# Optimization experiments

Measured on AMD Instinct MI355X. Metric: run time of the kernel, lower is better.

The kernel has to match this reference:

```python
import jax, jax.numpy as jnp
import numpy as np
from jax import lax

B, C, H, W = 8, 64, 96, 96
OC = 64
KH = KW = 3
DG = 1
STRIDE = 1
PAD = 1
DIL = 1


def setup_inputs() -> dict:
    key = jax.random.key(0)
    k1, k2, k3, k4, k5 = jax.random.split(key, 5)
    x = jax.random.normal(k1, (B, C, H, W), jnp.float32)
    off_ch = DG * 3 * KH * KW
    # small random offset/mask conv params (the original inits them to zero,
    # which would make offsets degenerate; small values exercise the sampler)
    w_off = jax.random.normal(k2, (off_ch, C, KH, KW), jnp.float32) * 0.01
    b_off = jax.random.normal(k3, (off_ch,), jnp.float32) * 0.01
    stdv = 1.0 / float(np.sqrt(C * KH * KW))
    weight = jax.random.uniform(k4, (OC, C, KH, KW), jnp.float32, -stdv, stdv)
    bias = jax.random.uniform(k5, (OC,), jnp.float32, -stdv, stdv)
    return {"x": x, "w_off": w_off, "b_off": b_off, "weight": weight, "bias": bias}


def _deform_conv(x, w_off, b_off, weight, bias):
    Bt, Ct, Ht, Wt = x.shape
    K = KH * KW
    # standard conv producing offsets + mask logits
    om = lax.conv_general_dilated(
        x, w_off, (STRIDE, STRIDE), ((PAD, PAD), (PAD, PAD)),
        rhs_dilation=(DIL, DIL), dimension_numbers=("NCHW", "OIHW", "NCHW"),
    ) + b_off[None, :, None, None]
    o1, o2, m = jnp.split(om, 3, axis=1)  # each [B, DG*K, Ho, Wo]
    Ho, Wo = o1.shape[2], o1.shape[3]
    mask = jax.nn.sigmoid(m).reshape(Bt, DG, 1, K, Ho, Wo)
    off_y = o1.reshape(Bt, DG, K, Ho, Wo)
    off_x = o2.reshape(Bt, DG, K, Ho, Wo)
    # base sampling grid: p = out_pos*stride - pad + k*dilation + offset
    kk = jnp.arange(K)
    base_y = (kk // KW)[:, None] * DIL + (jnp.arange(Ho) * STRIDE - PAD)[None, :]  # [K, Ho]
    base_x = (kk % KW)[:, None] * DIL + (jnp.arange(Wo) * STRIDE - PAD)[None, :]   # [K, Wo]
    py = off_y + base_y[None, None, :, :, None].astype(x.dtype)  # [B, DG, K, Ho, Wo]
    px = off_x + base_x[None, None, :, None, :].astype(x.dtype)
    y0 = jnp.floor(py)
    x0 = jnp.floor(px)
    ly = py - y0
    lx = px - x0
    Cg = Ct // DG
    xg = x.reshape(Bt, DG, Cg, Ht * Wt)

    def gath(xf, idx):  # xf [Cg, H*W], idx [K*Ho*Wo]
        return jnp.take(xf, idx, axis=1)

    gather = jax.vmap(jax.vmap(gath))  # over B, DG

    sampled = jnp.zeros((Bt, DG, Cg, K, Ho, Wo), x.dtype)
    for dy, dx, wgt in ((0, 0, (1 - ly) * (1 - lx)), (0, 1, (1 - ly) * lx),
                        (1, 0, ly * (1 - lx)), (1, 1, ly * lx)):
        yy = y0 + dy
        xx = x0 + dx
        valid = (yy >= 0) & (yy < Ht) & (xx >= 0) & (xx < Wt)
        yi = jnp.clip(yy, 0, Ht - 1).astype(jnp.int32)
        xi = jnp.clip(xx, 0, Wt - 1).astype(jnp.int32)
        idx = (yi * Wt + xi).reshape(Bt, DG, K * Ho * Wo)
        v = gather(xg, idx).reshape(Bt, DG, Cg, K, Ho, Wo)
        sampled = sampled + v * (wgt * valid)[:, :, None]
    sampled = sampled * mask  # modulated
    wr = weight.reshape(OC, DG, Cg, K)
    out = jnp.einsum("bgckhw,ogck->bohw", sampled, wr) + bias[None, :, None, None]
    return out


def reference(x, w_off, b_off, weight, bias):
    return _deform_conv(x, w_off, b_off, weight, bias)
```

## Files before the change

### kernel.cpp

```cpp
#include <hip/hip_runtime.h>
#include <math.h>

#define Bn 8
#define Cn 64
#define Hn 96
#define Wn 96
#define HWn (Hn*Wn)
#define OCn 64
#define Kn 9
#define OFFCn 27
#define NPIX (Bn*HWn)
#define PGRPS (NPIX/64)
#define BLK_PER_B (HWn/64)

#define WPK1_N 15552
#define WPK2M_SHORTS 131072
#define WS_DWORDS (WPK1_N + WPK2M_SHORTS/2)
#define WS_BYTES  ((size_t)WS_DWORDS*4)

typedef __attribute__((ext_vector_type(8))) short short8v;
typedef __attribute__((ext_vector_type(4))) float f32x4;

static __device__ __forceinline__ unsigned short bf16_rne(float f) {
    unsigned int u = __float_as_uint(f);
    return (unsigned short)((u + 0x7FFFu + ((u >> 16) & 1u)) >> 16);
}
static __device__ __forceinline__ float bf16_back(unsigned short h) {
    return __uint_as_float(((unsigned int)h) << 16);
}

__global__ __launch_bounds__(256) void dcn_wprep(
    const float* __restrict__ w_off,
    const float* __restrict__ weight,
    float* __restrict__ wpk1,
    short* __restrict__ wpk2m)
{
    const int g = blockIdx.x * 256 + threadIdx.x;
    if (g < WPK1_N) {
        const int c_all = g / 243;
        const int och   = (g % 243) / 9;
        const int ki    = g % 9;
        wpk1[g] = w_off[(och * 64 + c_all) * 9 + ki];
    }
    if (g < WPK2M_SHORTS / 8) {
        const int lane = g & 63;
        const int oct  = (g >> 6) & 3;
        const int c    = g >> 8;
        const int oc   = oct * 16 + (lane & 15);
        const float* wsrc = weight + (oc * 64 + c) * 9;
        short8v v;
#pragma unroll
        for (int j = 0; j < 8; ++j) {
            const int s = ((lane >> 4) & 3) * 8 + j;
            float f = 0.0f;
            if (s <= 8)                  f = wsrc[s];
            else if (s >= 16 && s <= 24) f = wsrc[s - 16];
            v[j] = (short)bf16_rne(f);
        }
        ((short8v*)wpk2m)[g] = v;
    }
}

__global__ __launch_bounds__(256, 2) void dcn_fused(
    const float* __restrict__ x,
    const float* __restrict__ wpk1,
    const float* __restrict__ b_off,
    const short* __restrict__ wpk2m,
    const float* __restrict__ bias,
    float* __restrict__ out)
{
    __shared__ short smp[32 * 64 * 8];
    float* lds1 = (float*)smp;

    const int tid  = threadIdx.x;
    const int lane = tid & 63;
    const int wv   = tid >> 6;
    const int cbase = __builtin_amdgcn_readfirstlane(wv * 16);

    const int bid = (blockIdx.x & 7) * BLK_PER_B + (blockIdx.x >> 3);

    const int p0  = bid * 64;
    const int b   = p0 / HWn;
    const int hwb = p0 % HWn;
    const int p   = p0 + lane;
    const int hw  = p % HWn;
    const int ho  = hw / Wn;
    const int wo  = hw % Wn;

    const float* xb = x + b * (Cn * HWn);

    float om[OFFCn];
    {
        int   toff[Kn];
        float tval[Kn];
#pragma unroll
        for (int ki = 0; ki < Kn; ++ki) {
            const int yy = ho + ki / 3 - 1, xx = wo + ki % 3 - 1;
            const bool v = (yy >= 0) && (yy < Hn) && (xx >= 0) && (xx < Wn);
            toff[ki] = min(max(yy, 0), Hn - 1) * Wn + min(max(xx, 0), Wn - 1);
            tval[ki] = v ? 1.0f : 0.0f;
        }

#pragma unroll
        for (int j = 0; j < OFFCn; ++j) om[j] = 0.0f;

        const float* wstream = wpk1 + cbase * 243;
        for (int ci = 0; ci < 16; ++ci) {
            const float* xc = xb + (cbase + ci) * HWn;
            float xk[Kn];
#pragma unroll
            for (int ki = 0; ki < Kn; ++ki)
                xk[ki] = xc[toff[ki]] * tval[ki];

            const float* wc = wstream + ci * 243;
#pragma unroll
            for (int och = 0; och < OFFCn; ++och) {
                const float* wp = wc + och * 9;
                float a = om[och];
#pragma unroll
                for (int ki = 0; ki < Kn; ++ki)
                    a = fmaf(xk[ki], wp[ki], a);
                om[och] = a;
            }
        }

#pragma unroll
        for (int j = 0; j < OFFCn; ++j)
            lds1[(wv * 64 + lane) * OFFCn + j] = om[j];
        __syncthreads();
#pragma unroll
        for (int j = 0; j < OFFCn; ++j) {
            float a = b_off[j];
#pragma unroll
            for (int ww = 0; ww < 4; ++ww)
                a += lds1[(ww * 64 + lane) * OFFCn + j];
            om[j] = a;
        }
    }

    float pw0[Kn], pw1[Kn], pw2[Kn], pw3[Kn];
    int   pav[Kn];
#pragma unroll
    for (int ki = 0; ki < Kn; ++ki) {
        const float py = om[ki]      + (float)(ki / 3 + ho - 1);
        const float px = om[Kn + ki] + (float)(ki % 3 + wo - 1);
        const float m  = 1.0f / (1.0f + __expf(-om[2 * Kn + ki]));

        const float y0f = floorf(py), x0f = floorf(px);
        const float ly = py - y0f, lx = px - x0f;
        const int iy0 = (int)y0f, ix0 = (int)x0f;
        const int iy1 = iy0 + 1,  ix1 = ix0 + 1;

        const float vy0 = (iy0 >= 0 && iy0 < Hn) ? 1.0f : 0.0f;
        const float vy1 = (iy1 >= 0 && iy1 < Hn) ? 1.0f : 0.0f;
        const float vx0 = (ix0 >= 0 && ix0 < Wn) ? 1.0f : 0.0f;
        const float vx1 = (ix1 >= 0 && ix1 < Wn) ? 1.0f : 0.0f;

        const int iy0c = min(max(iy0, 0), Hn - 1);
        const int iy1c = min(max(iy1, 0), Hn - 1);
        const int ix0c = min(max(ix0, 0), Wn - 1);
        const int ix1c = min(max(ix1, 0), Wn - 1);

        pw0[ki] = m * (1.0f - ly) * (1.0f - lx) * vy0 * vx0;
        pw1[ki] = m * (1.0f - ly) * lx          * vy0 * vx1;
        pw2[ki] = m * ly          * (1.0f - lx) * vy1 * vx0;
        pw3[ki] = m * ly          * lx          * vy1 * vx1;
        const int pa  = iy0c * Wn + ix0c;
        const int dx  = ix1c - ix0c;
        const int dyw = (iy1c - iy0c) * Wn;
        pav[ki] = pa | (dx << 16) | (dyw << 17);
    }
    __syncthreads();

    f32x4 acc[4];
#pragma unroll
    for (int oct = 0; oct < 4; ++oct) acc[oct] = (f32x4){0.f, 0.f, 0.f, 0.f};

    const short8v* afrags = (const short8v*)wpk2m;

    for (int chunk = 0; chunk < 8; ++chunk) {
#pragma unroll
        for (int cc = 0; cc < 2; ++cc) {
            const int cl = (wv << 1) | cc;
            const float* xc = xb + (chunk * 8 + cl) * HWn;
            unsigned short hi[Kn], lo[Kn];
#pragma unroll
            for (int ki = 0; ki < Kn; ++ki) {
                const int av  = pav[ki];
                const int pa  = av & 0xFFFF;
                const int dx  = (av >> 16) & 1;
                const int dyw = av >> 17;
                const float* bp = xc + pa;
                const float v = pw0[ki] * bp[0] + pw1[ki] * bp[dx]
                              + pw2[ki] * bp[dyw] + pw3[ki] * bp[dyw + dx];
                hi[ki] = bf16_rne(v);
                lo[ki] = bf16_rne(v - bf16_back(hi[ki]));
            }
            short8v h0, h1, l0, l1;
#pragma unroll
            for (int j = 0; j < 8; ++j) { h0[j] = (short)hi[j]; l0[j] = (short)lo[j]; }
            h1 = (short8v){(short)hi[8], 0, 0, 0, 0, 0, 0, 0};
            l1 = (short8v){(short)lo[8], 0, 0, 0, 0, 0, 0, 0};
            const int r0 = cl * 4;
            *(short8v*)&smp[((r0 + 0) * 64 + lane) * 8] = h0;
            *(short8v*)&smp[((r0 + 1) * 64 + lane) * 8] = h1;
            *(short8v*)&smp[((r0 + 2) * 64 + lane) * 8] = l0;
            *(short8v*)&smp[((r0 + 3) * 64 + lane) * 8] = l1;
        }
        __syncthreads();

#pragma unroll
        for (int ks = 0; ks < 8; ++ks) {
            const short8v bfrag = *(const short8v*)
                &smp[((ks * 4 + (lane >> 4)) * 64 + wv * 16 + (lane & 15)) * 8];
#pragma unroll
            for (int oct = 0; oct < 4; ++oct) {
                const short8v afrag =
                    afrags[(((chunk * 8 + ks) * 4) + oct) * 64 + lane];
                acc[oct] = __builtin_amdgcn_mfma_f32_16x16x32_bf16(
                    afrag, bfrag, acc[oct], 0, 0, 0);
            }
        }
        __syncthreads();
    }

    const int pxl = wv * 16 + (lane & 15);
    float* ob = out + b * (OCn * HWn) + hwb + pxl;
#pragma unroll
    for (int oct = 0; oct < 4; ++oct) {
#pragma unroll
        for (int r = 0; r < 4; ++r) {
            const int oc = oct * 16 + ((lane >> 4) & 3) * 4 + r;
            ob[oc * HWn] = acc[oct][r] + bias[oc];
        }
    }
}

__global__ __launch_bounds__(64) void dcn_r1(
    const float* __restrict__ x,
    const float* __restrict__ w_off,
    const float* __restrict__ b_off,
    const float* __restrict__ weight,
    const float* __restrict__ bias,
    float* __restrict__ out)
{
    const int p  = blockIdx.x * 64 + threadIdx.x;
    const int b  = p / HWn;
    const int hw = p % HWn;
    const int ho = hw / Wn;
    const int wo = hw % Wn;
    const float* xb = x + b * (Cn * HWn);

    float om[OFFCn];
#pragma unroll
    for (int j = 0; j < OFFCn; ++j) om[j] = b_off[j];

    int   toff[Kn];
    float tval[Kn];
#pragma unroll
    for (int ki = 0; ki < Kn; ++ki) {
        const int yy = ho + ki / 3 - 1, xx = wo + ki % 3 - 1;
        const bool v = (yy >= 0) && (yy < Hn) && (xx >= 0) && (xx < Wn);
        toff[ki] = min(max(yy, 0), Hn - 1) * Wn + min(max(xx, 0), Wn - 1);
        tval[ki] = v ? 1.0f : 0.0f;
    }
    for (int c = 0; c < Cn; ++c) {
        const float* xc = xb + c * HWn;
        float xk[Kn];
#pragma unroll
        for (int ki = 0; ki < Kn; ++ki) xk[ki] = xc[toff[ki]] * tval[ki];
        const float* wc = w_off + c * Kn;
#pragma unroll
        for (int och = 0; och < OFFCn; ++och) {
            const float* wp = wc + och * (Cn * Kn);
            float a = om[och];
#pragma unroll
            for (int ki = 0; ki < Kn; ++ki) a = fmaf(xk[ki], wp[ki], a);
            om[och] = a;
        }
    }
    float pw0[Kn], pw1[Kn], pw2[Kn], pw3[Kn];
    int   pa[Kn], pdx[Kn], pdyw[Kn];
#pragma unroll
    for (int ki = 0; ki < Kn; ++ki) {
        const float py = om[ki]      + (float)(ki / 3 + ho - 1);
        const float px = om[Kn + ki] + (float)(ki % 3 + wo - 1);
        const float m  = 1.0f / (1.0f + __expf(-om[2 * Kn + ki]));
        const float y0f = floorf(py), x0f = floorf(px);
        const float ly = py - y0f, lx = px - x0f;
        const int iy0 = (int)y0f, ix0 = (int)x0f;
        const int iy1 = iy0 + 1,  ix1 = ix0 + 1;
        const float vy0 = (iy0 >= 0 && iy0 < Hn) ? 1.0f : 0.0f;
        const float vy1 = (iy1 >= 0 && iy1 < Hn) ? 1.0f : 0.0f;
        const float vx0 = (ix0 >= 0 && ix0 < Wn) ? 1.0f : 0.0f;
        const float vx1 = (ix1 >= 0 && ix1 < Wn) ? 1.0f : 0.0f;
        const int iy0c = min(max(iy0, 0), Hn - 1);
        const int iy1c = min(max(iy1, 0), Hn - 1);
        const int ix0c = min(max(ix0, 0), Wn - 1);
        const int ix1c = min(max(ix1, 0), Wn - 1);
        pw0[ki] = m * (1.0f - ly) * (1.0f - lx) * vy0 * vx0;
        pw1[ki] = m * (1.0f - ly) * lx          * vy0 * vx1;
        pw2[ki] = m * ly          * (1.0f - lx) * vy1 * vx0;
        pw3[ki] = m * ly          * lx          * vy1 * vx1;
        pa[ki]   = iy0c * Wn + ix0c;
        pdx[ki]  = ix1c - ix0c;
        pdyw[ki] = (iy1c - iy0c) * Wn;
    }
    float acc[OCn];
#pragma unroll
    for (int oc = 0; oc < OCn; ++oc) acc[oc] = bias[oc];
    for (int c = 0; c < Cn; ++c) {
        const float* xc = xb + c * HWn;
        float s[Kn];
#pragma unroll
        for (int ki = 0; ki < Kn; ++ki) {
            const float* bp = xc + pa[ki];
            s[ki] = pw0[ki] * bp[0] + pw1[ki] * bp[pdx[ki]]
                  + pw2[ki] * bp[pdyw[ki]] + pw3[ki] * bp[pdyw[ki] + pdx[ki]];
        }
        const float* wc = weight + c * Kn;
#pragma unroll
        for (int oc = 0; oc < OCn; ++oc) {
            const float* wp = wc + oc * (Cn * Kn);
            float a = acc[oc];
#pragma unroll
            for (int ki = 0; ki < Kn; ++ki) a = fmaf(s[ki], wp[ki], a);
            acc[oc] = a;
        }
    }
    float* ob = out + b * (OCn * HWn) + hw;
#pragma unroll
    for (int oc = 0; oc < OCn; ++oc) ob[oc * HWn] = acc[oc];
}

extern "C" void kernel_launch(void* const* d_in, const int* in_sizes, int n_in,
                              void* d_out, int out_size, void* d_ws, size_t ws_size,
                              hipStream_t stream) {
    const float* x      = (const float*)d_in[0];
    const float* w_off  = (const float*)d_in[1];
    const float* b_off  = (const float*)d_in[2];
    const float* weight = (const float*)d_in[3];
    const float* bias   = (const float*)d_in[4];
    float* out = (float*)d_out;

    if (ws_size >= WS_BYTES) {
        float* wpk1  = (float*)d_ws;
        short* wpk2m = (short*)(wpk1 + WPK1_N);
        hipLaunchKernelGGL(dcn_wprep, dim3(64), dim3(256), 0, stream,
                           w_off, weight, wpk1, wpk2m);
        hipLaunchKernelGGL(dcn_fused, dim3(PGRPS), dim3(256), 0, stream,
                           x, wpk1, b_off, wpk2m, bias, out);
    } else {
        hipLaunchKernelGGL(dcn_r1, dim3(NPIX / 64), dim3(64), 0, stream,
                           x, w_off, b_off, weight, bias, out);
    }
}
```

Baseline: 237.7 us.

## Stage 12-row input window in LDS for offset conv and bilinear sampling

Each block now copies a 12-row window of eight input channels at a time into shared memory. Both the offset/mask convolution and the bilinear sampling read from this window instead of issuing scattered global loads. The offset conv is restructured so every wave handles two channels per chunk, with a sync per chunk. Sampling uses the LDS window only when every lane's sample falls inside it, otherwise it falls back to global reads. This adds about 36KB of LDS per block, which may reduce occupancy below the two blocks per CU the launch bounds ask for, and it adds extra barriers.

Measured after the change: 666.3 us. +180.3%, slower.

```diff
diff --git a/kernel.cpp b/kernel.cpp
--- a/kernel.cpp
+++ b/kernel.cpp
@@ -12,6 +12,8 @@
 #define NPIX (Bn*HWn)
 #define PGRPS (NPIX/64)
 #define BLK_PER_B (HWn/64)
+#define WROWS 12
+#define WPLANE (WROWS*Wn)
 
 #define WPK1_N 15552
 #define WPK2M_SHORTS 131072
@@ -69,13 +71,13 @@
     const float* __restrict__ bias,
     float* __restrict__ out)
 {
+    __shared__ float xstage[8 * WPLANE];
     __shared__ short smp[32 * 64 * 8];
     float* lds1 = (float*)smp;
 
     const int tid  = threadIdx.x;
     const int lane = tid & 63;
     const int wv   = tid >> 6;
-    const int cbase = __builtin_amdgcn_readfirstlane(wv * 16);
 
     const int bid = (blockIdx.x & 7) * BLK_PER_B + (blockIdx.x >> 3);
 
@@ -89,30 +91,47 @@
 
     const float* xb = x + b * (Cn * HWn);
 
+    const int r0   = hwb / Wn;
+    const int rw   = min(max(r0 - 4, 0), Hn - WROWS);
+    const int rw96 = rw * Wn;
+
+    const int sc = tid >> 5;
+    const int st = tid & 31;
+
+    int   ltoff[Kn];
+    float tval[Kn];
+#pragma unroll
+    for (int ki = 0; ki < Kn; ++ki) {
+        const int yy = ho + ki / 3 - 1, xx = wo + ki % 3 - 1;
+        const bool v = (yy >= 0) && (yy < Hn) && (xx >= 0) && (xx < Wn);
+        ltoff[ki] = min(max(yy, 0), Hn - 1) * Wn + min(max(xx, 0), Wn - 1) - rw96;
+        tval[ki] = v ? 1.0f : 0.0f;
+    }
+
     float om[OFFCn];
-    {
-        int   toff[Kn];
-        float tval[Kn];
-#pragma unroll
-        for (int ki = 0; ki < Kn; ++ki) {
-            const int yy = ho + ki / 3 - 1, xx = wo + ki % 3 - 1;
-            const bool v = (yy >= 0) && (yy < Hn) && (xx >= 0) && (xx < Wn);
-            toff[ki] = min(max(yy, 0), Hn - 1) * Wn + min(max(xx, 0), Wn - 1);
-            tval[ki] = v ? 1.0f : 0.0f;
-        }
-
-#pragma unroll
-        for (int j = 0; j < OFFCn; ++j) om[j] = 0.0f;
-
-        const float* wstream = wpk1 + cbase * 243;
-        for (int ci = 0; ci < 16; ++ci) {
-            const float* xc = xb + (cbase + ci) * HWn;
+#pragma unroll
+    for (int j = 0; j < OFFCn; ++j) om[j] = 0.0f;
+
+    for (int chunk = 0; chunk < 8; ++chunk) {
+        {
+            const float4* src = (const float4*)(xb + (chunk * 8 + sc) * HWn + rw96);
+            float4* dst = (float4*)(xstage + sc * WPLANE);
+#pragma unroll
+            for (int i = 0; i < 9; ++i) dst[st + 32 * i] = src[st + 32 * i];
+        }
+        __syncthreads();
+
+#pragma unroll
+        for (int cc = 0; cc < 2; ++cc) {
+            const int cl = wv * 2 + cc;
+            const int c  = chunk * 8 + cl;
+            const float* xs = xstage + cl * WPLANE;
             float xk[Kn];
 #pragma unroll
             for (int ki = 0; ki < Kn; ++ki)
-                xk[ki] = xc[toff[ki]] * tval[ki];
-
-            const float* wc = wstream + ci * 243;
+                xk[ki] = xs[ltoff[ki]] * tval[ki];
+
+            const float* wc = wpk1 + c * 243;
 #pragma unroll
             for (int och = 0; och < OFFCn; ++och) {
                 const float* wp = wc + och * 9;
@@ -123,23 +142,25 @@
                 om[och] = a;
             }
         }
-
-#pragma unroll
-        for (int j = 0; j < OFFCn; ++j)
-            lds1[(wv * 64 + lane) * OFFCn + j] = om[j];
         __syncthreads();
-#pragma unroll
-        for (int j = 0; j < OFFCn; ++j) {
-            float a = b_off[j];
-#pragma unroll
-            for (int ww = 0; ww < 4; ++ww)
-                a += lds1[(ww * 64 + lane) * OFFCn + j];
-            om[j] = a;
-        }
+    }
+
+#pragma unroll
+    for (int j = 0; j < OFFCn; ++j)
+        lds1[(wv * 64 + lane) * OFFCn + j] = om[j];
+    __syncthreads();
+#pragma unroll
+    for (int j = 0; j < OFFCn; ++j) {
+        float a = b_off[j];
+#pragma unroll
+        for (int ww = 0; ww < 4; ++ww)
+            a += lds1[(ww * 64 + lane) * OFFCn + j];
+        om[j] = a;
     }
 
     float pw0[Kn], pw1[Kn], pw2[Kn], pw3[Kn];
     int   pav[Kn];
+    int   okm = 0;
 #pragma unroll
     for (int ki = 0; ki < Kn; ++ki) {
         const float py = om[ki]      + (float)(ki / 3 + ho - 1);
@@ -169,6 +190,10 @@
         const int dx  = ix1c - ix0c;
         const int dyw = (iy1c - iy0c) * Wn;
         pav[ki] = pa | (dx << 16) | (dyw << 17);
+
+        const int lpa = pa - rw96;
+        const int ok  = (lpa >= 0) && (lpa + dyw + dx < WPLANE);
+        okm |= ok << ki;
     }
     __syncthreads();
 
@@ -177,37 +202,69 @@
     for (int oct = 0; oct < 4; ++oct) acc[oct] = (f32x4){0.f, 0.f, 0.f, 0.f};
 
     const short8v* afrags = (const short8v*)wpk2m;
+    const int fastpath = __all(okm == 0x1FF);
+
+    {
+        const float4* src = (const float4*)(xb + sc * HWn + rw96);
+        float4* dst = (float4*)(xstage + sc * WPLANE);
+#pragma unroll
+        for (int i = 0; i < 9; ++i) dst[st + 32 * i] = src[st + 32 * i];
+    }
+    __syncthreads();
 
     for (int chunk = 0; chunk < 8; ++chunk) {
 #pragma unroll
         for (int cc = 0; cc < 2; ++cc) {
             const int cl = (wv << 1) | cc;
-            const float* xc = xb + (chunk * 8 + cl) * HWn;
             unsigned short hi[Kn], lo[Kn];
-#pragma unroll
-            for (int ki = 0; ki < Kn; ++ki) {
-                const int av  = pav[ki];
-                const int pa  = av & 0xFFFF;
-                const int dx  = (av >> 16) & 1;
-                const int dyw = av >> 17;
-                const float* bp = xc + pa;
-                const float v = pw0[ki] * bp[0] + pw1[ki] * bp[dx]
-                              + pw2[ki] * bp[dyw] + pw3[ki] * bp[dyw + dx];
-                hi[ki] = bf16_rne(v);
-                lo[ki] = bf16_rne(v - bf16_back(hi[ki]));
+            if (fastpath) {
+                const float* xs = xstage + cl * WPLANE - rw96;
+#pragma unroll
+                for (int ki = 0; ki < Kn; ++ki) {
+                    const int av  = pav[ki];
+                    const int pa  = av & 0xFFFF;
+                    const int dx  = (av >> 16) & 1;
+                    const int dyw = av >> 17;
+                    const float* bp = xs + pa;
+                    const float v = pw0[ki] * bp[0] + pw1[ki] * bp[dx]
+                                  + pw2[ki] * bp[dyw] + pw3[ki] * bp[dyw + dx];
+                    hi[ki] = bf16_rne(v);
+                    lo[ki] = bf16_rne(v - bf16_back(hi[ki]));
+                }
+            } else {
+                const float* xc = xb + (chunk * 8 + cl) * HWn;
+#pragma unroll
+                for (int ki = 0; ki < Kn; ++ki) {
+                    const int av  = pav[ki];
+                    const int pa  = av & 0xFFFF;
+                    const int dx  = (av >> 16) & 1;
+                    const int dyw = av >> 17;
+                    const float* bp = xc + pa;
+                    const float v = pw0[ki] * bp[0] + pw1[ki] * bp[dx]
+                                  + pw2[ki] * bp[dyw] + pw3[ki] * bp[dyw + dx];
+                    hi[ki] = bf16_rne(v);
+                    lo[ki] = bf16_rne(v - bf16_back(hi[ki]));
+                }
             }
             short8v h0, h1, l0, l1;
 #pragma unroll
             for (int j = 0; j < 8; ++j) { h0[j] = (short)hi[j]; l0[j] = (short)lo[j]; }
             h1 = (short8v){(short)hi[8], 0, 0, 0, 0, 0, 0, 0};
             l1 = (short8v){(short)lo[8], 0, 0, 0, 0, 0, 0, 0};
-            const int r0 = cl * 4;
-            *(short8v*)&smp[((r0 + 0) * 64 + lane) * 8] = h0;
-            *(short8v*)&smp[((r0 + 1) * 64 + lane) * 8] = h1;
-            *(short8v*)&smp[((r0 + 2) * 64 + lane) * 8] = l0;
-            *(short8v*)&smp[((r0 + 3) * 64 + lane) * 8] = l1;
+            const int r0s = cl * 4;
+            *(short8v*)&smp[((r0s + 0) * 64 + lane) * 8] = h0;
+            *(short8v*)&smp[((r0s + 1) * 64 + lane) * 8] = h1;
+            *(short8v*)&smp[((r0s + 2) * 64 + lane) * 8] = l0;
+            *(short8v*)&smp[((r0s + 3) * 64 + lane) * 8] = l1;
         }
         __syncthreads();
+
+        if (chunk < 7) {
+            const float4* src = (const float4*)(xb + ((chunk + 1) * 8 + sc) * HWn + rw96);
+            float4* dst = (float4*)(xstage + sc * WPLANE);
+#pragma unroll
+            for (int i = 0; i < 9; ++i) dst[st + 32 * i] = src[st + 32 * i];
+        }
 
 #pragma unroll
         for (int ks = 0; ks < 8; ++ks) {
```

## Split fused DCN block across 8 waves instead of 4

Applied to the files above, without the earlier changes.

Doubles the fused kernel's block to 512 threads. Each wave now covers 8 input channels in the offset conv and one channel per chunk in the sampling stage, and the MFMA work is split so each wave handles 2 of the 4 output-channel tiles for one 16-pixel group. The offset partial sums are reduced in two LDS stages with extra barriers. The aim is more parallelism and latency hiding per block, in exchange for more syncs, duplicated bfrag reads, and tighter register limits from launch_bounds(512,4).

New measurement: 346.2 us. +45.6%, slower.

```diff
diff --git a/kernel.cpp b/kernel.cpp
--- a/kernel.cpp
+++ b/kernel.cpp
@@ -61,7 +61,7 @@
     }
 }
 
-__global__ __launch_bounds__(256, 2) void dcn_fused(
+__global__ __launch_bounds__(512, 4) void dcn_fused(
     const float* __restrict__ x,
     const float* __restrict__ wpk1,
     const float* __restrict__ b_off,
@@ -75,7 +75,6 @@
     const int tid  = threadIdx.x;
     const int lane = tid & 63;
     const int wv   = tid >> 6;
-    const int cbase = __builtin_amdgcn_readfirstlane(wv * 16);
 
     const int bid = (blockIdx.x & 7) * BLK_PER_B + (blockIdx.x >> 3);
 
@@ -104,8 +103,9 @@
 #pragma unroll
         for (int j = 0; j < OFFCn; ++j) om[j] = 0.0f;
 
+        const int cbase = __builtin_amdgcn_readfirstlane(wv * 8);
         const float* wstream = wpk1 + cbase * 243;
-        for (int ci = 0; ci < 16; ++ci) {
+        for (int ci = 0; ci < 8; ++ci) {
             const float* xc = xb + (cbase + ci) * HWn;
             float xk[Kn];
 #pragma unroll
@@ -124,9 +124,23 @@
             }
         }
 
-#pragma unroll
-        for (int j = 0; j < OFFCn; ++j)
-            lds1[(wv * 64 + lane) * OFFCn + j] = om[j];
+        if (wv >= 4) {
+#pragma unroll
+            for (int j = 0; j < OFFCn; ++j)
+                lds1[((wv - 4) * 64 + lane) * OFFCn + j] = om[j];
+        }
+        __syncthreads();
+        if (wv < 4) {
+#pragma unroll
+            for (int j = 0; j < OFFCn; ++j)
+                om[j] += lds1[(wv * 64 + lane) * OFFCn + j];
+        }
+        __syncthreads();
+        if (wv < 4) {
+#pragma unroll
+            for (int j = 0; j < OFFCn; ++j)
+                lds1[(wv * 64 + lane) * OFFCn + j] = om[j];
+        }
         __syncthreads();
 #pragma unroll
         for (int j = 0; j < OFFCn; ++j) {
@@ -172,17 +186,18 @@
     }
     __syncthreads();
 
-    f32x4 acc[4];
-#pragma unroll
-    for (int oct = 0; oct < 4; ++oct) acc[oct] = (f32x4){0.f, 0.f, 0.f, 0.f};
+    f32x4 acc[2];
+    acc[0] = (f32x4){0.f, 0.f, 0.f, 0.f};
+    acc[1] = (f32x4){0.f, 0.f, 0.f, 0.f};
 
     const short8v* afrags = (const short8v*)wpk2m;
+    const int pt = wv & 3;
+    const int oh = wv >> 2;
+    const int octA = oh * 2, octB = oh * 2 + 1;
 
     for (int chunk = 0; chunk < 8; ++chunk) {
-#pragma unroll
-        for (int cc = 0; cc < 2; ++cc) {
-            const int cl = (wv << 1) | cc;
-            const float* xc = xb + (chunk * 8 + cl) * HWn;
+        {
+            const float* xc = xb + (chunk * 8 + wv) * HWn;
             unsigned short hi[Kn], lo[Kn];
 #pragma unroll
             for (int ki = 0; ki < Kn; ++ki) {
@@ -201,7 +216,7 @@
             for (int j = 0; j < 8; ++j) { h0[j] = (short)hi[j]; l0[j] = (short)lo[j]; }
             h1 = (short8v){(short)hi[8], 0, 0, 0, 0, 0, 0, 0};
             l1 = (short8v){(short)lo[8], 0, 0, 0, 0, 0, 0, 0};
-            const int r0 = cl * 4;
+            const int r0 = wv * 4;
             *(short8v*)&smp[((r0 + 0) * 64 + lane) * 8] = h0;
             *(short8v*)&smp[((r0 + 1) * 64 + lane) * 8] = h1;
             *(short8v*)&smp[((r0 + 2) * 64 + lane) * 8] = l0;
@@ -212,26 +227,24 @@
 #pragma unroll
         for (int ks = 0; ks < 8; ++ks) {
             const short8v bfrag = *(const short8v*)
-                &smp[((ks * 4 + (lane >> 4)) * 64 + wv * 16 + (lane & 15)) * 8];
-#pragma unroll
-            for (int oct = 0; oct < 4; ++oct) {
-                const short8v afrag =
-                    afrags[(((chunk * 8 + ks) * 4) + oct) * 64 + lane];
-                acc[oct] = __builtin_amdgcn_mfma_f32_16x16x32_bf16(
-                    afrag, bfrag, acc[oct], 0, 0, 0);
-            }
-        }
-        __syncthreads();
-    }
-
-    const int pxl = wv * 16 + (lane & 15);
+                &smp[((ks * 4 + (lane >> 4)) * 64 + pt * 16 + (lane & 15)) * 8];
+            const short8v afA = afrags[(((chunk * 8 + ks) * 4) + octA) * 64 + lane];
+            const short8v afB = afrags[(((chunk * 8 + ks) * 4) + octB) * 64 + lane];
+            acc[0] = __builtin_amdgcn_mfma_f32_16x16x32_bf16(afA, bfrag, acc[0], 0, 0, 0);
+            acc[1] = __builtin_amdgcn_mfma_f32_16x16x32_bf16(afB, bfrag, acc[1], 0, 0, 0);
+        }
+        __syncthreads();
+    }
+
+    const int pxl = pt * 16 + (lane & 15);
     float* ob = out + b * (OCn * HWn) + hwb + pxl;
 #pragma unroll
-    for (int oct = 0; oct < 4; ++oct) {
+    for (int t = 0; t < 2; ++t) {
+        const int oct = oh * 2 + t;
 #pragma unroll
         for (int r = 0; r < 4; ++r) {
             const int oc = oct * 16 + ((lane >> 4) & 3) * 4 + r;
-            ob[oc * HWn] = acc[oct][r] + bias[oc];
+            ob[oc * HWn] = acc[t][r] + bias[oc];
         }
     }
 }
@@ -348,7 +361,7 @@
         short* wpk2m = (short*)(wpk1 + WPK1_N);
         hipLaunchKernelGGL(dcn_wprep, dim3(64), dim3(256), 0, stream,
                            w_off, weight, wpk1, wpk2m);
-        hipLaunchKernelGGL(dcn_fused, dim3(PGRPS), dim3(256), 0, stream,
+        hipLaunchKernelGGL(dcn_fused, dim3(PGRPS), dim3(512), 0, stream,
                            x, wpk1, b_off, wpk2m, bias, out);
     } else {
         hipLaunchKernelGGL(dcn_r1, dim3(NPIX / 64), dim3(64), 0, stream,
```

## Halve block to two waves, reuse weight fragments across two pixel tiles

Applied to the files above, without the earlier changes.

Shrinks the fused block from four waves to two, so each wave accumulates two 16-pixel MFMA tiles and reuses each weight fragment twice. The offset conv is split across two waves of 32 channels, with a two-step LDS reduction. This is meant to cut weight-fragment loads and LDS usage per block and to allow more resident blocks. In exchange, each wave does more serial work and uses more accumulator registers, which risks spills or lower latency hiding.

Result: slower. 491.0 us (+106.5%).

```diff
diff --git a/kernel.cpp b/kernel.cpp
--- a/kernel.cpp
+++ b/kernel.cpp
@@ -61,7 +61,7 @@
     }
 }
 
-__global__ __launch_bounds__(256, 2) void dcn_fused(
+__global__ __launch_bounds__(128, 4) void dcn_fused(
     const float* __restrict__ x,
     const float* __restrict__ wpk1,
     const float* __restrict__ b_off,
@@ -69,13 +69,12 @@
     const float* __restrict__ bias,
     float* __restrict__ out)
 {
-    __shared__ short smp[32 * 64 * 8];
+    __shared__ short smp[16 * 64 * 8];
     float* lds1 = (float*)smp;
 
     const int tid  = threadIdx.x;
     const int lane = tid & 63;
     const int wv   = tid >> 6;
-    const int cbase = __builtin_amdgcn_readfirstlane(wv * 16);
 
     const int bid = (blockIdx.x & 7) * BLK_PER_B + (blockIdx.x >> 3);
 
@@ -104,8 +103,9 @@
 #pragma unroll
         for (int j = 0; j < OFFCn; ++j) om[j] = 0.0f;
 
+        const int cbase = __builtin_amdgcn_readfirstlane(wv * 32);
         const float* wstream = wpk1 + cbase * 243;
-        for (int ci = 0; ci < 16; ++ci) {
+        for (int ci = 0; ci < 32; ++ci) {
             const float* xc = xb + (cbase + ci) * HWn;
             float xk[Kn];
 #pragma unroll
@@ -124,18 +124,21 @@
             }
         }
 
+        if (wv == 1) {
+#pragma unroll
+            for (int j = 0; j < OFFCn; ++j)
+                lds1[lane * OFFCn + j] = om[j];
+        }
+        __syncthreads();
+        if (wv == 0) {
+#pragma unroll
+            for (int j = 0; j < OFFCn; ++j)
+                lds1[lane * OFFCn + j] = om[j] + lds1[lane * OFFCn + j] + b_off[j];
+        }
+        __syncthreads();
 #pragma unroll
         for (int j = 0; j < OFFCn; ++j)
-            lds1[(wv * 64 + lane) * OFFCn + j] = om[j];
-        __syncthreads();
-#pragma unroll
-        for (int j = 0; j < OFFCn; ++j) {
-            float a = b_off[j];
-#pragma unroll
-            for (int ww = 0; ww < 4; ++ww)
-                a += lds1[(ww * 64 + lane) * OFFCn + j];
-            om[j] = a;
-        }
+            om[j] = lds1[lane * OFFCn + j];
     }
 
     float pw0[Kn], pw1[Kn], pw2[Kn], pw3[Kn];
@@ -172,17 +175,20 @@
     }
     __syncthreads();
 
-    f32x4 acc[4];
-#pragma unroll
-    for (int oct = 0; oct < 4; ++oct) acc[oct] = (f32x4){0.f, 0.f, 0.f, 0.f};
+    f32x4 acc[2][4];
+#pragma unroll
+    for (int t = 0; t < 2; ++t)
+#pragma unroll
+        for (int oct = 0; oct < 4; ++oct)
+            acc[t][oct] = (f32x4){0.f, 0.f, 0.f, 0.f};
 
     const short8v* afrags = (const short8v*)wpk2m;
 
-    for (int chunk = 0; chunk < 8; ++chunk) {
+    for (int chunk = 0; chunk < 16; ++chunk) {
 #pragma unroll
         for (int cc = 0; cc < 2; ++cc) {
             const int cl = (wv << 1) | cc;
-            const float* xc = xb + (chunk * 8 + cl) * HWn;
+            const float* xc = xb + (chunk * 4 + cl) * HWn;
             unsigned short hi[Kn], lo[Kn];
 #pragma unroll
             for (int ki = 0; ki < Kn; ++ki) {
@@ -210,28 +216,33 @@
         __syncthreads();
 
 #pragma unroll
-        for (int ks = 0; ks < 8; ++ks) {
-            const short8v bfrag = *(const short8v*)
-                &smp[((ks * 4 + (lane >> 4)) * 64 + wv * 16 + (lane & 15)) * 8];
+        for (int ks = 0; ks < 4; ++ks) {
+            const int c = chunk * 4 + ks;
+            const short8v bf0 = *(const short8v*)
+                &smp[((ks * 4 + (lane >> 4)) * 64 + (2 * wv) * 16 + (lane & 15)) * 8];
+            const short8v bf1 = *(const short8v*)
+                &smp[((ks * 4 + (lane >> 4)) * 64 + (2 * wv + 1) * 16 + (lane & 15)) * 8];
 #pragma unroll
             for (int oct = 0; oct < 4; ++oct) {
-                const short8v afrag =
-                    afrags[(((chunk * 8 + ks) * 4) + oct) * 64 + lane];
-                acc[oct] = __builtin_amdgcn_mfma_f32_16x16x32_bf16(
-                    afrag, bfrag, acc[oct], 0, 0, 0);
+                const short8v af = afrags[((c * 4) + oct) * 64 + lane];
+                acc[0][oct] = __builtin_amdgcn_mfma_f32_16x16x32_bf16(af, bf0, acc[0][oct], 0, 0, 0);
+                acc[1][oct] = __builtin_amdgcn_mfma_f32_16x16x32_bf16(af, bf1, acc[1][oct], 0, 0, 0);
             }
         }
         __syncthreads();
     }
 
-    const int pxl = wv * 16 + (lane & 15);
-    float* ob = out + b * (OCn * HWn) + hwb + pxl;
-#pragma unroll
-    for (int oct = 0; oct < 4; ++oct) {
-#pragma unroll
-        for (int r = 0; r < 4; ++r) {
-            const int oc = oct * 16 + ((lane >> 4) & 3) * 4 + r;
-            ob[oc * HWn] = acc[oct][r] + bias[oc];
+#pragma unroll
+    for (int t = 0; t < 2; ++t) {
+        const int pxl = (2 * wv + t) * 16 + (lane & 15);
+        float* ob = out + b * (OCn * HWn) + hwb + pxl;
+#pragma unroll
+        for (int oct = 0; oct < 4; ++oct) {
+#pragma unroll
+            for (int r = 0; r < 4; ++r) {
+                const int oc = oct * 16 + ((lane >> 4) & 3) * 4 + r;
+                ob[oc * HWn] = acc[t][oct][r] + bias[oc];
+            }
         }
     }
 }
@@ -348,7 +359,7 @@
         short* wpk2m = (short*)(wpk1 + WPK1_N);
         hipLaunchKernelGGL(dcn_wprep, dim3(64), dim3(256), 0, stream,
                            w_off, weight, wpk1, wpk2m);
-        hipLaunchKernelGGL(dcn_fused, dim3(PGRPS), dim3(256), 0, stream,
+        hipLaunchKernelGGL(dcn_fused, dim3(PGRPS), dim3(128), 0, stream,
                            x, wpk1, b_off, wpk2m, bias, out);
     } else {
         hipLaunchKernelGGL(dcn_r1, dim3(NPIX / 64), dim3(64), 0, stream,
```
